# Optimization experiments

Hardware: AMD Instinct MI355X
Metric: run time of the kernel (lower is better)

## Reference

```python
import jax, jax.numpy as jnp
import numpy as np

N = 16384
C = 4        # in_channels
K = 16       # neighbors
H = 64       # mlp width


def setup_inputs() -> dict:
    key = jax.random.key(0)
    k0, k1, k2, k3, k4 = jax.random.split(key, 5)
    x = jax.random.normal(k0, (N, C), dtype=jnp.float32)
    # nn.Linear(2C, 64) and nn.Linear(64, 64): weight [out, in], bias [out]
    W1 = jax.random.normal(k1, (H, 2 * C), dtype=jnp.float32) * (1.0 / np.sqrt(2 * C))
    b1 = jax.random.normal(k2, (H,), dtype=jnp.float32) * 0.01
    W2 = jax.random.normal(k3, (H, H), dtype=jnp.float32) * (1.0 / np.sqrt(H))
    b2 = jax.random.normal(k4, (H,), dtype=jnp.float32) * 0.01
    return {"x": x, "W1": W1, "b1": b1, "W2": W2, "b2": b2}


def reference(x, W1, b1, W2, b2):
    # x: [N, C] single point cloud (torch code unsqueezes batch dim 0)
    xs = jax.lax.stop_gradient(x)  # knn indices computed under no_grad
    # pairwise = -||xi - xj||^2 = 2*xi.xj - ||xi||^2 - ||xj||^2
    xx = jnp.sum(xs * xs, axis=1)                      # [N]
    pairwise = 2.0 * (xs @ xs.T) - xx[:, None] - xx[None, :]  # [N, N]
    _, idx = jax.lax.top_k(pairwise, K)                # [N, K] (self included, dist 0 is max)
    neigh = x[idx]                                     # [N, K, C] gather
    center = jnp.broadcast_to(x[:, None, :], (x.shape[0], K, C))
    edge = jnp.concatenate([neigh - center, center], axis=-1)  # [N, K, 2C]
    h = jax.nn.relu(jnp.einsum('nkc,hc->nkh', edge, W1) + b1)
    h = jax.nn.relu(jnp.einsum('nkh,gh->nkg', h, W2) + b2)     # [N, K, H]
    out = jnp.mean(h, axis=1)                          # [N, H]
    return out[None]                                   # [1, N, H] matches torch output
```

## Files before the change

kernel.cpp:

```cpp
#include <hip/hip_runtime.h>
#include <math.h>

#define N_PTS 16384
#define K_NBR 16
#define H_DIM 64
#define QPB   32
#define CAP   38
#define NBLK  (N_PTS / 16)
#define HBLK  (NBLK / 2)
#define PBLK  (HBLK / 4)

typedef unsigned long long u64;
typedef unsigned short u16;
typedef float v2f   __attribute__((ext_vector_type(2)));
typedef float f32x4 __attribute__((ext_vector_type(4)));
typedef short bf16x8 __attribute__((ext_vector_type(8)));

__device__ __forceinline__ u64 mkkey(unsigned vbits, unsigned idx) {
    unsigned of = vbits ^ (unsigned)(((int)vbits >> 31) | 0x80000000);
    return ((u64)of << 32) | (unsigned)(~idx);
}
__device__ __forceinline__ unsigned keyidx(u64 k) { return ~(unsigned)k; }

__device__ __forceinline__ float readlane_f(float v, int l) {
    return __uint_as_float(__builtin_amdgcn_readlane(__float_as_uint(v), l));
}

__device__ __forceinline__ unsigned ofsbits(float f) {
    unsigned b = __float_as_uint(f);
    return b ^ ((unsigned)((int)b >> 31) | 0x80000000u);
}
__device__ __forceinline__ float inv_ofs(unsigned u) {
    return __uint_as_float(u ^ (~(unsigned)((int)u >> 31) | 0x80000000u));
}

__device__ __forceinline__ u16 f2bf(float f) {
    unsigned u = __float_as_uint(f);
    return (u16)((u + 0x7FFFu + ((u >> 16) & 1u)) >> 16);
}
__device__ __forceinline__ float bf2f(u16 b) {
    return __uint_as_float(((unsigned)b) << 16);
}

__device__ __forceinline__ float wave_sort_f32(float v, int lane) {
#pragma unroll
    for (int k = 2; k <= 64; k <<= 1) {
#pragma unroll
        for (int j = k >> 1; j > 0; j >>= 1) {
            float o = __shfl_xor(v, j, 64);
            bool keep_min = (((lane & k) == 0) == ((lane & j) == 0));
            v = keep_min ? fminf(v, o) : fmaxf(v, o);
        }
    }
    return v;
}
__device__ __forceinline__ u64 wave_sort_u64(u64 v, int lane) {
#pragma unroll
    for (int k = 2; k <= 64; k <<= 1) {
#pragma unroll
        for (int j = k >> 1; j > 0; j >>= 1) {
            u64 o = __shfl_xor((unsigned long long)v, j, 64);
            bool keep_min = (((lane & k) == 0) == ((lane & j) == 0));
            u64 mn = (v < o) ? v : o;
            u64 mx = (v < o) ? o : v;
            v = keep_min ? mn : mx;
        }
    }
    return v;
}
__device__ __forceinline__ u64 half32_sort_u64(u64 v, int lane) {
    const int l = lane & 31;
#pragma unroll
    for (int k = 2; k <= 32; k <<= 1) {
#pragma unroll
        for (int j = k >> 1; j > 0; j >>= 1) {
            u64 o = __shfl_xor((unsigned long long)v, j, 64);
            bool keep_min = (((l & k) == 0) == ((l & j) == 0));
            u64 mn = (v < o) ? v : o;
            u64 mx = (v < o) ? o : v;
            v = keep_min ? mn : mx;
        }
    }
    return v;
}

struct CompRes { int nc; float tau; };
__device__ __attribute__((noinline)) CompRes wave_compact(uint2* buf, int cnt,
                                                          int lane) {
    float lm = -INFINITY;
    for (int s = lane; s < cnt; s += 64)
        lm = fmaxf(lm, __uint_as_float(buf[s].x));
    const float tv = readlane_f(wave_sort_f32(lm, lane), 48);
    int nc = 0;
    for (int s0 = 0; s0 < cnt; s0 += 64) {
        const int s = s0 + lane;
        uint2 e = make_uint2(0u, 0u);
        bool keep = false;
        if (s < cnt) { e = buf[s]; keep = (__uint_as_float(e.x) >= tv); }
        const u64 km = __ballot(keep);
        if (keep) {
            int pfx = (int)__popcll(km & ((1ull << lane) - 1));
            buf[nc + pfx] = e;
        }
        nc += (int)__popcll(km);
    }
    CompRes r; r.nc = nc; r.tau = tv;
    return r;
}

__device__ __forceinline__ bf16x8 make_qfrag(float4 xi, int g) {
    u16 Ha[4], Ma[4], La[4];
    float yy[4] = {2.f * xi.x, 2.f * xi.y, 2.f * xi.z, 2.f * xi.w};
#pragma unroll
    for (int c = 0; c < 4; ++c) {
        u16 h = f2bf(yy[c]);             float fh = bf2f(h);
        u16 m = f2bf(yy[c] - fh);        float fm = bf2f(m);
        u16 l = f2bf(yy[c] - fh - fm);
        Ha[c] = h; Ma[c] = m; La[c] = l;
    }
    const u16 ONEB = 0x3F80;
    bf16x8 qf;
#pragma unroll
    for (int c = 0; c < 4; ++c) {
        u16 lo, hi;
        if (g == 0)      { lo = Ha[c]; hi = Ha[c]; }
        else if (g == 1) { lo = Ma[c]; hi = Ha[c]; }
        else if (g == 2) { lo = La[c]; hi = Ma[c]; }
        else             { lo = (c < 3) ? ONEB : 0; hi = 0; }
        qf[c]     = (short)lo;
        qf[c + 4] = (short)hi;
    }
    return qf;
}

__global__ __launch_bounds__(256) void prep_kernel(const float4* __restrict__ x4,
                                                   u16* __restrict__ bf) {
    const int i = blockIdx.x * 256 + threadIdx.x;
    const float4 v = x4[i];
    float xx;
    {
#pragma clang fp contract(off)
        float s0 = v.x * v.x, s1 = v.y * v.y, s2 = v.z * v.z, s3 = v.w * v.w;
        xx = ((s0 + s1) + s2) + s3;
    }
    float c[4] = {v.x, v.y, v.z, v.w};
    u16 H[4], M[4], L[4];
#pragma unroll
    for (int q = 0; q < 4; ++q) {
        float f = c[q];
        u16 h = f2bf(f);            float fh = bf2f(h);
        u16 m = f2bf(f - fh);       float fm = bf2f(m);
        u16 l = f2bf(f - fh - fm);
        H[q] = h; M[q] = m; L[q] = l;
    }
    const float nx = -xx;
    u16 X0 = f2bf(nx);              float x0f = bf2f(X0);
    u16 X1 = f2bf(nx - x0f);        float x1f = bf2f(X1);
    u16 X2 = f2bf(nx - x0f - x1f);
    u16 o[32];
#pragma unroll
    for (int q = 0; q < 4; ++q) {
        o[q]      = H[q];
        o[4 + q]  = M[q];
        o[8 + q]  = H[q];
        o[12 + q] = L[q];
        o[16 + q] = H[q];
        o[20 + q] = M[q];
    }
    o[24] = X0; o[25] = X1; o[26] = X2;
    o[27] = 0; o[28] = 0; o[29] = 0; o[30] = 0; o[31] = 0;
    uint4* dst = (uint4*)(bf + (size_t)i * 32);
#pragma unroll
    for (int q2 = 0; q2 < 4; ++q2) {
        uint4 w;
        w.x = (unsigned)o[q2 * 8 + 0] | ((unsigned)o[q2 * 8 + 1] << 16);
        w.y = (unsigned)o[q2 * 8 + 2] | ((unsigned)o[q2 * 8 + 3] << 16);
        w.z = (unsigned)o[q2 * 8 + 4] | ((unsigned)o[q2 * 8 + 5] << 16);
        w.w = (unsigned)o[q2 * 8 + 6] | ((unsigned)o[q2 * 8 + 7] << 16);
        dst[q2] = w;
    }
}

__global__ __launch_bounds__(256, 4) void knn_kernel(
        const float4* __restrict__ x4,
        const u16* __restrict__ bfrag,
        unsigned* __restrict__ vals,
        u16* __restrict__ idxs) {
    __shared__ __align__(16) uint2 buf[4][QPB][CAP];
    __shared__ unsigned tau_sh[QPB];
    const int lane = threadIdx.x & 63;
    const int wave = threadIdx.x >> 6;
    const int q    = lane & 15;
    const int g    = lane >> 4;
    const int qgrp = blockIdx.x >> 1;
    const int half = blockIdx.x & 1;
    const int qbase = qgrp * QPB;
    const int pblk = half * HBLK + wave * PBLK;

    const bf16x8 qf0 = make_qfrag(x4[qbase + q], g);
    const bf16x8 qf1 = make_qfrag(x4[qbase + 16 + q], g);
    const f32x4 zacc = {0.f, 0.f, 0.f, 0.f};
    const bf16x8* bp = (const bf16x8*)bfrag + (size_t)pblk * 64 + (q * 4 + g);

    f32x4 mx0 = {-INFINITY, -INFINITY, -INFINITY, -INFINITY};
    f32x4 mx1 = mx0;
    for (int t = 0; t < PBLK; t += 8) {
        bf16x8 A0[4];
#pragma unroll
        for (int i = 0; i < 4; ++i) A0[i] = bp[(t + 2 * i) * 64];
#pragma unroll
        for (int i = 0; i < 4; ++i) {
            const f32x4 a0 = __builtin_amdgcn_mfma_f32_16x16x32_bf16(
                A0[i], qf0, zacc, 0, 0, 0);
            mx0[0] = fmaxf(mx0[0], a0[0]); mx0[1] = fmaxf(mx0[1], a0[1]);
            mx0[2] = fmaxf(mx0[2], a0[2]); mx0[3] = fmaxf(mx0[3], a0[3]);
            const f32x4 a1 = __builtin_amdgcn_mfma_f32_16x16x32_bf16(
                A0[i], qf1, zacc, 0, 0, 0);
            mx1[0] = fmaxf(mx1[0], a1[0]); mx1[1] = fmaxf(mx1[1], a1[1]);
            mx1[2] = fmaxf(mx1[2], a1[2]); mx1[3] = fmaxf(mx1[3], a1[3]);
        }
    }

    {
        float* am = (float*)&buf[0][0][0];
        const int col = wave * 16 + g * 4;
#pragma unroll
        for (int j = 0; j < 4; ++j) {
            am[q * 64 + col + j]        = mx0[j];
            am[(16 + q) * 64 + col + j] = mx1[j];
        }
        __syncthreads();
#pragma unroll
        for (int rr = 0; rr < 8; ++rr) {
            const int r = wave * 8 + rr;
            float v = am[r * 64 + lane];
            v = wave_sort_f32(v, lane);
            if (lane == 48) tau_sh[r] = ofsbits(v);
        }
        __syncthreads();
    }
    float tau0 = inv_ofs(tau_sh[q]);
    float tau1 = inv_ofs(tau_sh[16 + q]);

    unsigned cq0 = 0, cq1 = 0;
    uint2* bq0 = &buf[wave][q][0];
    uint2* bq1 = &buf[wave][16 + q][0];
    const unsigned gid4 = (unsigned)(g * 4);

#define INSERT4(AV, CB, TAU, CQ, BQ, ROWOFF) do {                            \
    for (;;) {                                                               \
        const bool k0 = (AV)[0] >= (TAU), k1 = (AV)[1] >= (TAU);             \
        const bool k2 = (AV)[2] >= (TAU), k3 = (AV)[3] >= (TAU);             \
        const int cnt = (int)k0 + (int)k1 + (int)k2 + (int)k3;               \
        const int sa = __shfl_xor(cnt, 16, 64);                              \
        const int sb = __shfl_xor(cnt, 32, 64);                              \
        const int sc = __shfl_xor(sa, 32, 64);                               \
        const int tot = cnt + sa + sb + sc;                                  \
        const int pf  = ((g & 1) ? sa : 0) + ((g & 2) ? (sb + sc) : 0);      \
        const u64 ovm = __ballot((CQ) + (unsigned)tot > CAP);                \
        if (__builtin_expect(ovm == 0, 1)) {                                 \
            unsigned slot = (CQ) + (unsigned)pf;                             \
            if (k0) (BQ)[slot++] = make_uint2(__float_as_uint((AV)[0]), (CB)); \
            if (k1) (BQ)[slot++] = make_uint2(__float_as_uint((AV)[1]), (CB)+1);\
            if (k2) (BQ)[slot++] = make_uint2(__float_as_uint((AV)[2]), (CB)+2);\
            if (k3) (BQ)[slot++] = make_uint2(__float_as_uint((AV)[3]), (CB)+3);\
            (CQ) += (unsigned)tot;                                           \
            break;                                                           \
        }                                                                    \
        u64 ov = ovm & 0xFFFFull;                                            \
        while (ov) {                                                         \
            const int r = (int)__builtin_ctzll(ov); ov &= ov - 1;            \
            const unsigned cr =                                              \
                (unsigned)__builtin_amdgcn_readlane((int)(CQ), r);           \
            CompRes res = wave_compact(&buf[wave][(ROWOFF) + r][0], (int)cr, \
                                       lane);                                \
            if (q == r) { (CQ) = (unsigned)res.nc;                           \
                          (TAU) = fmaxf((TAU), res.tau); }                   \
        }                                                                    \
    }                                                                        \
} while (0)

#define PROC4(BUF, TB) do {                                                  \
    _Pragma("unroll")                                                        \
    for (int i = 0; i < 4; ++i) {                                            \
        const f32x4 a0 = __builtin_amdgcn_mfma_f32_16x16x32_bf16(            \
            BUF[i], qf0, zacc, 0, 0, 0);                                     \
        const f32x4 a1 = __builtin_amdgcn_mfma_f32_16x16x32_bf16(            \
            BUF[i], qf1, zacc, 0, 0, 0);                                     \
        const unsigned cb = (unsigned)(((TB) + i) * 16) + gid4;              \
        const float m0 = fmaxf(fmaxf(a0[0], a0[1]), fmaxf(a0[2], a0[3]));    \
        if (__ballot(m0 >= tau0)) INSERT4(a0, cb, tau0, cq0, bq0, 0);        \
        const float m1 = fmaxf(fmaxf(a1[0], a1[1]), fmaxf(a1[2], a1[3]));    \
        if (__ballot(m1 >= tau1)) INSERT4(a1, cb, tau1, cq1, bq1, 16);       \
    }                                                                        \
} while (0)

    {
        bf16x8 B0[4], B1[4];
#pragma unroll
        for (int i = 0; i < 4; ++i) B0[i] = bp[i * 64];
#pragma unroll
        for (int i = 0; i < 4; ++i) B1[i] = bp[(4 + i) * 64];
        const bf16x8* pA = bp + 8 * 64;
        const bf16x8* pB = bp + 12 * 64;

        int t = 0;
        for (; t < PBLK - 8; t += 8) {
            PROC4(B0, pblk + t);
#pragma unroll
            for (int i = 0; i < 4; ++i) B0[i] = pA[i * 64];
            pA += 8 * 64;
            PROC4(B1, pblk + t + 4);
#pragma unroll
            for (int i = 0; i < 4; ++i) B1[i] = pB[i * 64];
            pB += 8 * 64;
        }
        PROC4(B0, pblk + t);
        PROC4(B1, pblk + t + 4);
    }
#undef PROC4
#undef INSERT4

#pragma unroll 1
    for (int r = 0; r < QPB; ++r) {
        int c = __builtin_amdgcn_readlane((int)((r < 16) ? cq0 : cq1), r & 15);
        uint2* br = &buf[wave][r][0];
        if (c <= 16) {
            if (lane < 16) {
                u64 key = 0;
                if (lane < c) { const uint2 e = br[lane]; key = mkkey(e.x, e.y); }
                *(u64*)&buf[wave][r][lane] = key;
            }
        } else {
            u64 key = 0;
            if (lane < c) { const uint2 e = br[lane]; key = mkkey(e.x, e.y); }
            key = wave_sort_u64(key, lane);
            if (lane >= 48)
                *(u64*)&buf[wave][r][lane - 48] = key;
        }
    }

    __syncthreads();
#pragma unroll
    for (int rr = 0; rr < 8; ++rr) {
        const int r2 = wave * 8 + rr;
        u64 key = *(const u64*)&buf[lane >> 4][r2][lane & 15];
        key = wave_sort_u64(key, lane);
        if (lane >= 48) {
            const int o = (qbase + r2) * 32 + half * 16 + (lane - 48);
            vals[o] = (unsigned)(key >> 32);
            idxs[o] = (u16)keyidx(key);
        }
    }
}

__global__ __launch_bounds__(256, 2) void mlp_kernel(
        const float4* __restrict__ x4,
        const unsigned* __restrict__ vals,
        const u16* __restrict__ idxs,
        const float4* __restrict__ W2f4,
        const float* __restrict__ W1,
        const float* __restrict__ b1,
        const float* __restrict__ b2,
        float* __restrict__ out) {
    __shared__ __align__(16) float4 w2s[16][64];
    __shared__ __align__(16) float  h1s[4][32][68];
    __shared__ __align__(16) float4 xjs[4][32];
    const int lane = threadIdx.x & 63;
    const int wave = threadIdx.x >> 6;
    const int kq   = lane >> 4;
    const int gp   = lane & 15;
    const int p0   = (blockIdx.x * 4 + wave) * 2;

    for (int q = threadIdx.x; q < 1024; q += 256)
        w2s[q & 15][q >> 4] = W2f4[q];
    __syncthreads();

    float w1r[8];
#pragma unroll
    for (int c = 0; c < 8; ++c) w1r[c] = W1[lane * 8 + c];
    const float b1r = b1[lane];
    float b2r[4];
#pragma unroll
    for (int gq = 0; gq < 4; ++gq) b2r[gq] = b2[gq * 16 + gp];

    {
        const int pp = lane >> 5;
        const int j  = lane & 31;
        const int o  = (p0 + pp) * 32 + j;
        u64 key = ((u64)vals[o] << 32) | (unsigned)(~(unsigned)idxs[o]);
        key = half32_sort_u64(key, lane);
        if ((lane & 31) >= 16) {
            const int nb = (int)((~(unsigned)key) & 0xFFFFu);
            xjs[wave][pp * 16 + ((lane & 31) - 16)] = x4[nb];
        }
    }

#pragma unroll
    for (int pp = 0; pp < 2; ++pp) {
        const float4 xi = x4[p0 + pp];
        float hb = b1r;
        hb = fmaf(w1r[4] - w1r[0], xi.x, hb);
        hb = fmaf(w1r[5] - w1r[1], xi.y, hb);
        hb = fmaf(w1r[6] - w1r[2], xi.z, hb);
        hb = fmaf(w1r[7] - w1r[3], xi.w, hb);
#pragma unroll
        for (int k = 0; k < K_NBR; ++k) {
            const float4 xj = xjs[wave][pp * 16 + k];
            float h = hb;
            h = fmaf(w1r[0], xj.x, h);
            h = fmaf(w1r[1], xj.y, h);
            h = fmaf(w1r[2], xj.z, h);
            h = fmaf(w1r[3], xj.w, h);
            h1s[wave][pp * 16 + k][lane] = fmaxf(h, 0.0f);
        }
    }

    v2f acc[2][4][4];
#pragma unroll
    for (int pp = 0; pp < 2; ++pp)
#pragma unroll
        for (int kk = 0; kk < 4; ++kk)
#pragma unroll
            for (int gq = 0; gq < 4; ++gq)
                acc[pp][kk][gq] = (v2f){b2r[gq], 0.0f};

#pragma unroll
    for (int h4 = 0; h4 < 16; ++h4) {
        float4 w4[4];
#pragma unroll
        for (int gq = 0; gq < 4; ++gq) w4[gq] = w2s[h4][gq * 16 + gp];
#pragma unroll
        for (int pp = 0; pp < 2; ++pp) {
#pragma unroll
            for (int kk = 0; kk < 4; ++kk) {
                const float4 hv =
                    *(const float4*)&h1s[wave][pp * 16 + kq * 4 + kk][h4 * 4];
#pragma unroll
                for (int gq = 0; gq < 4; ++gq) {
                    acc[pp][kk][gq] = __builtin_elementwise_fma(
                        (v2f){hv.x, hv.y}, (v2f){w4[gq].x, w4[gq].y},
                        acc[pp][kk][gq]);
                    acc[pp][kk][gq] = __builtin_elementwise_fma(
                        (v2f){hv.z, hv.w}, (v2f){w4[gq].z, w4[gq].w},
                        acc[pp][kk][gq]);
                }
            }
        }
    }

#pragma unroll
    for (int pp = 0; pp < 2; ++pp) {
        float s[4];
#pragma unroll
        for (int gq = 0; gq < 4; ++gq) {
            s[gq] = 0.0f;
#pragma unroll
            for (int kk = 0; kk < 4; ++kk) {
                const float v = acc[pp][kk][gq].x + acc[pp][kk][gq].y;
                s[gq] += fmaxf(v, 0.0f);
            }
        }
#pragma unroll
        for (int off = 16; off <= 32; off <<= 1)
#pragma unroll
            for (int gq = 0; gq < 4; ++gq)
                s[gq] += __shfl_xor(s[gq], off, 64);

        out[(p0 + pp) * H_DIM + kq * 16 + gp] = s[kq] * (1.0f / 16.0f);
    }
}

extern "C" void kernel_launch(void* const* d_in, const int* in_sizes, int n_in,
                              void* d_out, int out_size, void* d_ws, size_t ws_size,
                              hipStream_t stream) {
    (void)in_sizes; (void)n_in; (void)out_size; (void)ws_size;
    const float* x  = (const float*)d_in[0];
    const float* W1 = (const float*)d_in[1];
    const float* b1 = (const float*)d_in[2];
    const float* W2 = (const float*)d_in[3];
    const float* b2 = (const float*)d_in[4];
    float* out = (float*)d_out;

    u16*      bfrag = (u16*)d_ws;
    unsigned* vals  = (unsigned*)((char*)d_ws + (1u << 20));
    u16*      idxs  = (u16*)((char*)d_ws + (3u << 20));

    const float4* x4 = (const float4*)x;

    prep_kernel<<<N_PTS / 256, 256, 0, stream>>>(x4, bfrag);
    knn_kernel <<<N_PTS / QPB * 2, 256, 0, stream>>>(x4, bfrag, vals, idxs);
    mlp_kernel <<<N_PTS / 8,   256, 0, stream>>>(
        x4, vals, idxs, (const float4*)W2, W1, b1, b2, out);
}
```

Before: 204.7 us.

## Process one point per wave in MLP kernel, read W2 from global

```diff
diff --git a/kernel.cpp b/kernel.cpp
--- a/kernel.cpp
+++ b/kernel.cpp
@@ -354,7 +354,7 @@
     }
 }
 
-__global__ __launch_bounds__(256, 2) void mlp_kernel(
+__global__ __launch_bounds__(256, 4) void mlp_kernel(
         const float4* __restrict__ x4,
         const unsigned* __restrict__ vals,
         const u16* __restrict__ idxs,
@@ -363,18 +363,13 @@
         const float* __restrict__ b1,
         const float* __restrict__ b2,
         float* __restrict__ out) {
-    __shared__ __align__(16) float4 w2s[16][64];
-    __shared__ __align__(16) float  h1s[4][32][68];
-    __shared__ __align__(16) float4 xjs[4][32];
+    __shared__ __align__(16) float  h1s[4][16][68];
+    __shared__ __align__(16) float4 xjs[4][16];
     const int lane = threadIdx.x & 63;
     const int wave = threadIdx.x >> 6;
     const int kq   = lane >> 4;
     const int gp   = lane & 15;
-    const int p0   = (blockIdx.x * 4 + wave) * 2;
-
-    for (int q = threadIdx.x; q < 1024; q += 256)
-        w2s[q & 15][q >> 4] = W2f4[q];
-    __syncthreads();
+    const int p    = blockIdx.x * 4 + wave;
 
     float w1r[8];
 #pragma unroll
@@ -385,20 +380,18 @@
     for (int gq = 0; gq < 4; ++gq) b2r[gq] = b2[gq * 16 + gp];
 
     {
-        const int pp = lane >> 5;
-        const int j  = lane & 31;
-        const int o  = (p0 + pp) * 32 + j;
+        const int j = lane & 31;
+        const int o = p * 32 + j;
         u64 key = ((u64)vals[o] << 32) | (unsigned)(~(unsigned)idxs[o]);
         key = half32_sort_u64(key, lane);
-        if ((lane & 31) >= 16) {
+        if (lane >= 16 && lane < 32) {
             const int nb = (int)((~(unsigned)key) & 0xFFFFu);
-            xjs[wave][pp * 16 + ((lane & 31) - 16)] = x4[nb];
-        }
-    }
-
-#pragma unroll
-    for (int pp = 0; pp < 2; ++pp) {
-        const float4 xi = x4[p0 + pp];
+            xjs[wave][lane - 16] = x4[nb];
+        }
+    }
+
+    {
+        const float4 xi = x4[p];
         float hb = b1r;
         hb = fmaf(w1r[4] - w1r[0], xi.x, hb);
         hb = fmaf(w1r[5] - w1r[1], xi.y, hb);
@@ -406,58 +399,53 @@
         hb = fmaf(w1r[7] - w1r[3], xi.w, hb);
 #pragma unroll
         for (int k = 0; k < K_NBR; ++k) {
-            const float4 xj = xjs[wave][pp * 16 + k];
+            const float4 xj = xjs[wave][k];
             float h = hb;
             h = fmaf(w1r[0], xj.x, h);
             h = fmaf(w1r[1], xj.y, h);
             h = fmaf(w1r[2], xj.z, h);
             h = fmaf(w1r[3], xj.w, h);
-            h1s[wave][pp * 16 + k][lane] = fmaxf(h, 0.0f);
-        }
-    }
-
-    v2f acc[2][4][4];
-#pragma unroll
-    for (int pp = 0; pp < 2; ++pp)
-#pragma unroll
-        for (int kk = 0; kk < 4; ++kk)
-#pragma unroll
-            for (int gq = 0; gq < 4; ++gq)
-                acc[pp][kk][gq] = (v2f){b2r[gq], 0.0f};
-
+            h1s[wave][k][lane] = fmaxf(h, 0.0f);
+        }
+    }
+
+    v2f acc[4][4];
+#pragma unroll
+    for (int kk = 0; kk < 4; ++kk)
+#pragma unroll
+        for (int gq = 0; gq < 4; ++gq)
+            acc[kk][gq] = (v2f){b2r[gq], 0.0f};
+
+    const float4* w2row = W2f4 + gp * 16;
 #pragma unroll
     for (int h4 = 0; h4 < 16; ++h4) {
         float4 w4[4];
 #pragma unroll
-        for (int gq = 0; gq < 4; ++gq) w4[gq] = w2s[h4][gq * 16 + gp];
-#pragma unroll
-        for (int pp = 0; pp < 2; ++pp) {
-#pragma unroll
-            for (int kk = 0; kk < 4; ++kk) {
-                const float4 hv =
-                    *(const float4*)&h1s[wave][pp * 16 + kq * 4 + kk][h4 * 4];
-#pragma unroll
-                for (int gq = 0; gq < 4; ++gq) {
-                    acc[pp][kk][gq] = __builtin_elementwise_fma(
-                        (v2f){hv.x, hv.y}, (v2f){w4[gq].x, w4[gq].y},
-                        acc[pp][kk][gq]);
-                    acc[pp][kk][gq] = __builtin_elementwise_fma(
-                        (v2f){hv.z, hv.w}, (v2f){w4[gq].z, w4[gq].w},
-                        acc[pp][kk][gq]);
-                }
+        for (int gq = 0; gq < 4; ++gq) w4[gq] = w2row[gq * 256 + h4];
+#pragma unroll
+        for (int kk = 0; kk < 4; ++kk) {
+            const float4 hv =
+                *(const float4*)&h1s[wave][kq * 4 + kk][h4 * 4];
+#pragma unroll
+            for (int gq = 0; gq < 4; ++gq) {
+                acc[kk][gq] = __builtin_elementwise_fma(
+                    (v2f){hv.x, hv.y}, (v2f){w4[gq].x, w4[gq].y},
+                    acc[kk][gq]);
+                acc[kk][gq] = __builtin_elementwise_fma(
+                    (v2f){hv.z, hv.w}, (v2f){w4[gq].z, w4[gq].w},
+                    acc[kk][gq]);
             }
         }
     }
 
-#pragma unroll
-    for (int pp = 0; pp < 2; ++pp) {
+    {
         float s[4];
 #pragma unroll
         for (int gq = 0; gq < 4; ++gq) {
             s[gq] = 0.0f;
 #pragma unroll
             for (int kk = 0; kk < 4; ++kk) {
-                const float v = acc[pp][kk][gq].x + acc[pp][kk][gq].y;
+                const float v = acc[kk][gq].x + acc[kk][gq].y;
                 s[gq] += fmaxf(v, 0.0f);
             }
         }
@@ -467,7 +455,7 @@
             for (int gq = 0; gq < 4; ++gq)
                 s[gq] += __shfl_xor(s[gq], off, 64);
 
-        out[(p0 + pp) * H_DIM + kq * 16 + gp] = s[kq] * (1.0f / 16.0f);
+        out[p * H_DIM + kq * 16 + gp] = s[kq] * (1.0f / 16.0f);
     }
 }
 
@@ -490,6 +478,6 @@
 
     prep_kernel<<<N_PTS / 256, 256, 0, stream>>>(x4, bfrag);
     knn_kernel <<<N_PTS / QPB * 2, 256, 0, stream>>>(x4, bfrag, vals, idxs);
-    mlp_kernel <<<N_PTS / 8,   256, 0, stream>>>(
+    mlp_kernel <<<N_PTS / 4,   256, 0, stream>>>(
         x4, vals, idxs, (const float4*)W2, W1, b1, b2, out);
 }
```

Result: slower. 294.2 us (+43.7%).
